# Kernel tuning notes

Measured on AMD Instinct MI355X. Metric: run time of the kernel, lower is better.

Reference implementation:

```python
import jax, jax.numpy as jnp
import numpy as np

L_RTN = 3  # complex taps produced by the RTN head (w_rtn3 out dim = 2*L_RTN)
EPS = 1e-12


def _to_complex(x):
    # (B, 2n) real interleaved [re0, im0, re1, im1, ...] -> (B, n) complex
    return x[:, 0::2] + 1j * x[:, 1::2]


def _to_real(xc):
    # (B, n) complex -> (B, 2n) real interleaved
    b, n = xc.shape
    return jnp.stack([xc.real, xc.imag], axis=-1).reshape(b, 2 * n)


def _complex_conv_taps(h_c, x_c):
    # per-sample causal complex FIR: out[t] = sum_l h[l] * x[t-l]
    # h_c: (B, L) complex, x_c: (B, n) complex
    n = x_c.shape[1]
    out = jnp.zeros_like(x_c)
    for l in range(h_c.shape[1]):  # L is tiny and static
        shifted = jnp.pad(x_c, ((0, 0), (l, 0)))[:, :n]
        out = out + h_c[:, l:l + 1] * shifted
    return out


def setup_inputs() -> dict:
    key = jax.random.key(0)
    ks = jax.random.split(key, 16)
    B, D_IN, H1, CH, H_RTN, H2, D_OUT = 8192, 512, 4096, 256, 1024, 4096, 512
    s = 0.02  # weight init scale
    x = jax.random.normal(ks[0], (B, D_IN), jnp.float32)
    w1 = s * jax.random.normal(ks[1], (H1, D_IN), jnp.float32)
    b1 = jnp.zeros((H1,), jnp.float32)
    w2 = s * jax.random.normal(ks[2], (CH, H1), jnp.float32)
    b2 = jnp.zeros((CH,), jnp.float32)
    w_rtn1 = s * jax.random.normal(ks[3], (H_RTN, CH), jnp.float32)
    b_rtn1 = jnp.zeros((H_RTN,), jnp.float32)
    w_rtn2 = s * jax.random.normal(ks[4], (H_RTN, H_RTN), jnp.float32)
    b_rtn2 = jnp.zeros((H_RTN,), jnp.float32)
    w_rtn3 = s * jax.random.normal(ks[5], (2 * L_RTN, H_RTN), jnp.float32)
    # bias so that RTN starts near identity tap [1, 0, 0, ...]
    b_rtn3 = jnp.zeros((2 * L_RTN,), jnp.float32).at[0].set(1.0)
    w3 = s * jax.random.normal(ks[6], (H2, CH), jnp.float32)
    b3 = jnp.zeros((H2,), jnp.float32)
    w4 = s * jax.random.normal(ks[7], (D_OUT, H2), jnp.float32)
    b4 = jnp.zeros((D_OUT,), jnp.float32)
    h = jax.random.normal(ks[8], (2,), jnp.float32)
    h = h / jnp.linalg.norm(h)  # unit-power single-tap fading channel
    noise = 0.1 * jax.random.normal(ks[9], (B, CH), jnp.float32)
    return {"x": x, "w1": w1, "b1": b1, "w2": w2, "b2": b2,
            "w_rtn1": w_rtn1, "b_rtn1": b_rtn1, "w_rtn2": w_rtn2,
            "b_rtn2": b_rtn2, "w_rtn3": w_rtn3, "b_rtn3": b_rtn3,
            "w3": w3, "b3": b3, "w4": w4, "b4": b4, "h": h, "noise": noise}


def reference(x, w1, b1, w2, b2, w_rtn1, b_rtn1, w_rtn2, b_rtn2,
              w_rtn3, b_rtn3, w3, b3, w4, b4, h, noise):
    # encoder (linear1 -> relu -> linear2)
    a = jax.nn.relu(x @ w1.T + b1)
    s = a @ w2.T + b2                      # (B, 2n) channel signal
    # power normalization: sqrt(2n) * sqrt(0.5) * s / ||s||
    scale = jnp.sqrt(s.shape[1] * 0.5)
    s = scale * s / jnp.linalg.norm(s, axis=1, keepdims=True)
    tx_c = _to_complex(s)                  # (B, n) transmitted symbols
    # single-tap complex channel
    h_c = h[0] + 1j * h[1]
    y = _to_real(h_c * tx_c) + noise       # add per-sample AWGN
    y_c = _to_complex(y)
    # LS channel estimate (1 tap): h_est = <y, x> / <x, x>
    num = jnp.sum(y_c * jnp.conj(tx_c), axis=1, keepdims=True)
    den = jnp.sum(jnp.abs(tx_c) ** 2, axis=1, keepdims=True)
    h_est = num / den                      # (B, 1)
    # zero-forcing signal estimate
    x_eq = y_c * jnp.conj(h_est) / (jnp.abs(h_est) ** 2 + EPS)
    xr = _to_real(x_eq)                    # (B, 2n)
    # RTN: predict inverse taps and apply per-sample complex conv
    g = jnp.tanh(xr @ w_rtn1.T + b_rtn1)
    g = jnp.tanh(g @ w_rtn2.T + b_rtn2)
    h_inv = g @ w_rtn3.T + b_rtn3          # (B, 2*L_RTN)
    h_inv_c = h_inv[:, 0::2] + 1j * h_inv[:, 1::2]
    xr = _to_real(_complex_conv_taps(h_inv_c, _to_complex(xr)))
    # decoder (linear3 -> relu -> linear4)
    out = jax.nn.relu(xr @ w3.T + b3)
    return out @ w4.T + b4
```

## Files before the change

### kernel.cpp

```cpp
#include <hip/hip_runtime.h>
#include <hip/hip_bf16.h>
#include <math.h>

using bf16 = __hip_bfloat16;
typedef __attribute__((ext_vector_type(8))) short short8;
typedef __attribute__((ext_vector_type(4))) float float4v;

template <typename T> __device__ inline T cvt_out(float v);
template <> __device__ inline float cvt_out<float>(float v) { return v; }
template <> __device__ inline bf16 cvt_out<bf16>(float v) { return __float2bfloat16(v); }

__device__ inline void gload_lds16(const bf16* g, bf16* l) {
    __builtin_amdgcn_global_load_lds(
        (const __attribute__((address_space(1))) void*)g,
        (__attribute__((address_space(3))) void*)l, 16, 0, 0);
}

struct CvtPack {
    const float* src[7];
    bf16* dst[7];
    int end[7];
};

__global__ __launch_bounds__(256) void cvt_all(CvtPack p) {
    int e = (blockIdx.x * 256 + threadIdx.x) * 4;
    int start = 0;
#pragma unroll
    for (int s = 0; s < 7; ++s) {
        if (e < p.end[s]) {
            int off = e - start;
            float4 v = *(const float4*)(p.src[s] + off);
            bf16* d = p.dst[s] + off;
            d[0] = __float2bfloat16(v.x);
            d[1] = __float2bfloat16(v.y);
            d[2] = __float2bfloat16(v.z);
            d[3] = __float2bfloat16(v.w);
            return;
        }
        start = p.end[s];
    }
}

template <int NK>
__global__ __launch_bounds__(256) void reduceK_bias(const float* __restrict__ p,
                                                    const float* __restrict__ bias,
                                                    float* __restrict__ out,
                                                    size_t mn, int nmask, int total4) {
    int i = blockIdx.x * 256 + threadIdx.x;
    if (i < total4) {
        int idx = i * 4;
        float4 bb = *(const float4*)(bias + (idx & nmask));
        float4 r = bb;
#pragma unroll
        for (int k = 0; k < NK; ++k) {
            float4 a = *(const float4*)(p + k * mn + idx);
            r.x += a.x; r.y += a.y; r.z += a.z; r.w += a.w;
        }
        *(float4*)(out + idx) = r;
    }
}

template <int ACT, typename OutT, int WMT, int WNT, int BKT, bool PARTIAL>
__global__ __launch_bounds__(256) void gemm_bt(const bf16* __restrict__ A,
                                               const bf16* __restrict__ W,
                                               const float* __restrict__ bias,
                                               OutT* __restrict__ C,
                                               int M, int N, int K,
                                               int nbn, int kcount) {
    constexpr int TBM = 32 * WMT;
    constexpr int TBN = 32 * WNT;
    constexpr int CPR = BKT / 8;
    constexpr int CA = TBM * CPR;
    constexpr int CB = TBN * CPR;
    constexpr int STAGE_B = (TBM + TBN) * BKT * 2;
    constexpr int REPACK_B = TBM * TBN * (int)sizeof(OutT);
    constexpr int SH = STAGE_B > REPACK_B ? STAGE_B : REPACK_B;

    __shared__ __align__(16) char smem[SH];
    bf16* As = (bf16*)smem;
    bf16* Bs = As + TBM * BKT;

    const int bi = blockIdx.x;
    const int xcd = bi & 7, t = bi >> 3;
    const int bn = t % nbn;
    const int bm = xcd + 8 * (t / nbn);
    const int kbeg = PARTIAL ? blockIdx.y * kcount : 0;
    OutT* Cp = PARTIAL ? C + (size_t)blockIdx.y * M * N : C;

    const int tid = threadIdx.x;
    const int wave = tid >> 6, lane = tid & 63;
    const int wm = (wave >> 1) * (16 * WMT), wn = (wave & 1) * (16 * WNT);
    const int quad = lane >> 4, lrow = lane & 15;

    float4v acc[WMT][WNT] = {};
    const size_t arow = (size_t)(bm * TBM) * K;
    const size_t brow = (size_t)(bn * TBN) * K;

    for (int k0 = kbeg; k0 < kbeg + kcount; k0 += BKT) {
        __syncthreads();
#pragma unroll
        for (int tt = 0; tt < CA / 256; ++tt) {
            int base = tt * 256 + wave * 64;
            int c = base + lane;
            int row = c / CPR, col = (c % CPR) * 8;
            gload_lds16(A + arow + (size_t)row * K + k0 + col, As + base * 8);
        }
#pragma unroll
        for (int tt = 0; tt < CB / 256; ++tt) {
            int base = tt * 256 + wave * 64;
            int c = base + lane;
            int row = c / CPR, col = (c % CPR) * 8;
            gload_lds16(W + brow + (size_t)row * K + k0 + col, Bs + base * 8);
        }
        __syncthreads();
#pragma unroll
        for (int kk = 0; kk < BKT; kk += 32) {
            short8 af[WMT], bfr[WNT];
#pragma unroll
            for (int i = 0; i < WMT; ++i)
                af[i] = *(const short8*)(As + (wm + i * 16 + lrow) * BKT + kk + quad * 8);
#pragma unroll
            for (int j = 0; j < WNT; ++j)
                bfr[j] = *(const short8*)(Bs + (wn + j * 16 + lrow) * BKT + kk + quad * 8);
#pragma unroll
            for (int i = 0; i < WMT; ++i)
#pragma unroll
                for (int j = 0; j < WNT; ++j)
                    acc[i][j] = __builtin_amdgcn_mfma_f32_16x16x32_bf16(af[i], bfr[j], acc[i][j], 0, 0, 0);
        }
    }

    __syncthreads();
    OutT* R = (OutT*)smem;
#pragma unroll
    for (int i = 0; i < WMT; ++i) {
        int row0 = wm + i * 16 + quad * 4;
#pragma unroll
        for (int j = 0; j < WNT; ++j) {
            int col = wn + j * 16 + lrow;
            float bv = 0.f;
            if constexpr (!PARTIAL) bv = bias[bn * TBN + col];
#pragma unroll
            for (int r = 0; r < 4; ++r) {
                float v = acc[i][j][r] + bv;
                if constexpr (!PARTIAL) {
                    if (ACT == 1) v = fmaxf(v, 0.f);
                    else if (ACT == 2) v = tanhf(v);
                }
                R[(row0 + r) * TBN + col] = cvt_out<OutT>(v);
            }
        }
    }
    __syncthreads();
    constexpr int EPC = 16 / (int)sizeof(OutT);
    constexpr int CR = TBN / EPC;
    constexpr int TOT = TBM * CR;
#pragma unroll
    for (int t2 = 0; t2 < TOT / 256; ++t2) {
        int c = t2 * 256 + tid;
        int row = c / CR, cin = c % CR;
        float4 v = *((const float4*)smem + c);
        *(float4*)&Cp[(size_t)(bm * TBM + row) * N + bn * TBN + cin * EPC] = v;
    }
}

__global__ __launch_bounds__(64) void channel_kernel(const float* __restrict__ s,
                                                     const float* __restrict__ h,
                                                     const float* __restrict__ noise,
                                                     float* __restrict__ xr_f,
                                                     bf16* __restrict__ xr_b) {
    const int b = blockIdx.x, lane = threadIdx.x;
    const float* srow = s + (size_t)b * 256;

    float ss = 0.f;
#pragma unroll
    for (int t = 0; t < 4; ++t) {
        float v = srow[lane + 64 * t];
        ss += v * v;
    }
#pragma unroll
    for (int off = 32; off; off >>= 1) ss += __shfl_xor(ss, off);
    const float inv = sqrtf(128.0f) / sqrtf(ss);

    const float hre = h[0], him = h[1];

    float yre[2], yim[2];
    float nre = 0.f, nim = 0.f, den = 0.f;
#pragma unroll
    for (int t = 0; t < 2; ++t) {
        int c = lane + 64 * t;
        float tr = srow[2 * c] * inv, ti = srow[2 * c + 1] * inv;
        float yr = hre * tr - him * ti + noise[(size_t)b * 256 + 2 * c];
        float yi = hre * ti + him * tr + noise[(size_t)b * 256 + 2 * c + 1];
        yre[t] = yr; yim[t] = yi;
        nre += yr * tr + yi * ti;
        nim += yi * tr - yr * ti;
        den += tr * tr + ti * ti;
    }
#pragma unroll
    for (int off = 32; off; off >>= 1) {
        nre += __shfl_xor(nre, off);
        nim += __shfl_xor(nim, off);
        den += __shfl_xor(den, off);
    }
    const float her = nre / den, hei = nim / den;
    const float d2 = her * her + hei * hei + 1e-12f;

#pragma unroll
    for (int t = 0; t < 2; ++t) {
        int c = lane + 64 * t;
        float xre = (yre[t] * her + yim[t] * hei) / d2;
        float xim = (yim[t] * her - yre[t] * hei) / d2;
        xr_f[(size_t)b * 256 + 2 * c] = xre;
        xr_f[(size_t)b * 256 + 2 * c + 1] = xim;
        xr_b[(size_t)b * 256 + 2 * c] = __float2bfloat16(xre);
        xr_b[(size_t)b * 256 + 2 * c + 1] = __float2bfloat16(xim);
    }
}

__global__ __launch_bounds__(64) void rtn_taps_conv(const bf16* __restrict__ g2,
                                                    const float* __restrict__ wr3,
                                                    const float* __restrict__ br3,
                                                    const float* __restrict__ xr_f,
                                                    bf16* __restrict__ xr2) {
    const int b = blockIdx.x, lane = threadIdx.x;
    const bf16* grow = g2 + (size_t)b * 1024;

    float acc[6] = {0.f, 0.f, 0.f, 0.f, 0.f, 0.f};
#pragma unroll
    for (int t = 0; t < 16; ++t) {
        int k = lane + 64 * t;
        float gv = __bfloat162float(grow[k]);
#pragma unroll
        for (int j = 0; j < 6; ++j) acc[j] += gv * wr3[j * 1024 + k];
    }
#pragma unroll
    for (int j = 0; j < 6; ++j)
#pragma unroll
        for (int off = 32; off; off >>= 1) acc[j] += __shfl_xor(acc[j], off);

    float tre[3], tim[3];
#pragma unroll
    for (int l = 0; l < 3; ++l) {
        tre[l] = acc[2 * l] + br3[2 * l];
        tim[l] = acc[2 * l + 1] + br3[2 * l + 1];
    }

    const float* xrow = xr_f + (size_t)b * 256;
#pragma unroll
    for (int t = 0; t < 2; ++t) {
        int c = lane + 64 * t;
        float ore = 0.f, oim = 0.f;
#pragma unroll
        for (int l = 0; l < 3; ++l) {
            int cc = c - l;
            if (cc >= 0) {
                float xre = xrow[2 * cc], xim = xrow[2 * cc + 1];
                ore += tre[l] * xre - tim[l] * xim;
                oim += tre[l] * xim + tim[l] * xre;
            }
        }
        xr2[(size_t)b * 256 + 2 * c] = __float2bfloat16(ore);
        xr2[(size_t)b * 256 + 2 * c + 1] = __float2bfloat16(oim);
    }
}

extern "C" void kernel_launch(void* const* d_in, const int* in_sizes, int n_in,
                              void* d_out, int out_size, void* d_ws, size_t ws_size,
                              hipStream_t stream) {
    constexpr int B = 8192, D_IN = 512, H1 = 4096, CH = 256, HR = 1024, H2 = 4096, DOUT = 512;

    const float* x   = (const float*)d_in[0];
    const float* w1  = (const float*)d_in[1];
    const float* b1  = (const float*)d_in[2];
    const float* w2  = (const float*)d_in[3];
    const float* b2  = (const float*)d_in[4];
    const float* wr1 = (const float*)d_in[5];
    const float* br1 = (const float*)d_in[6];
    const float* wr2 = (const float*)d_in[7];
    const float* br2 = (const float*)d_in[8];
    const float* wr3 = (const float*)d_in[9];
    const float* br3 = (const float*)d_in[10];
    const float* w3  = (const float*)d_in[11];
    const float* b3  = (const float*)d_in[12];
    const float* w4  = (const float*)d_in[13];
    const float* b4  = (const float*)d_in[14];
    const float* h   = (const float*)d_in[15];
    const float* noise = (const float*)d_in[16];

    char* ws = (char*)d_ws;
    bf16*  a    = (bf16*)(ws + 0);
    bf16*  g1   = (bf16*)(ws + 0);
    bf16*  g2   = (bf16*)(ws + 16777216);
    bf16*  tbuf = (bf16*)(ws + 0);
    bf16*  w1B  = (bf16*)(ws + 67108864);
    bf16*  w2B  = (bf16*)(ws + 71303168);
    bf16*  wr1B = (bf16*)(ws + 73400320);
    bf16*  wr2B = (bf16*)(ws + 73924608);
    bf16*  w3B  = (bf16*)(ws + 76021760);
    bf16*  w4B  = (bf16*)(ws + 78118912);
    bf16*  xB   = (bf16*)(ws + 82313216);
    float* sF   = (float*)(ws + 90701824);
    float* xrF  = (float*)(ws + 99090432);
    bf16*  xrB  = (bf16*)(ws + 107479040);
    bf16*  xr2  = (bf16*)(ws + 111673344);

    float* g2P = (float*)(ws + 82313216);
    float* g6P = (float*)(ws + 82313216);

    dim3 blk(256);

    CvtPack p;
    const float* srcs[7] = {x, w1, w2, wr1, wr2, w3, w4};
    bf16* dsts[7] = {xB, w1B, w2B, wr1B, wr2B, w3B, w4B};
    int ns[7] = {B * D_IN, H1 * D_IN, CH * H1, HR * CH, HR * HR, H2 * CH, DOUT * H2};
    int cum = 0;
    for (int i = 0; i < 7; ++i) { p.src[i] = srcs[i]; p.dst[i] = dsts[i]; cum += ns[i]; p.end[i] = cum; }
    cvt_all<<<(cum / 4 + 255) / 256, blk, 0, stream>>>(p);

    gemm_bt<1, bf16, 4, 4, 64, false><<<64 * 32, blk, 0, stream>>>(
        xB, w1B, b1, a, B, H1, D_IN, 32, D_IN);
    gemm_bt<0, float, 4, 2, 64, true><<<dim3(64 * 4, 4), blk, 0, stream>>>(
        a, w2B, nullptr, g2P, B, CH, H1, 4, H1 / 4);
    reduceK_bias<4><<<(B * CH / 4 + 255) / 256, blk, 0, stream>>>(
        g2P, b2, sF, (size_t)B * CH, CH - 1, B * CH / 4);
    channel_kernel<<<B, 64, 0, stream>>>(sF, h, noise, xrF, xrB);
    gemm_bt<2, bf16, 4, 2, 64, false><<<64 * 16, blk, 0, stream>>>(
        xrB, wr1B, br1, g1, B, HR, CH, 16, CH);
    gemm_bt<2, bf16, 4, 2, 64, false><<<64 * 16, blk, 0, stream>>>(
        g1, wr2B, br2, g2, B, HR, HR, 16, HR);
    rtn_taps_conv<<<B, 64, 0, stream>>>(g2, wr3, br3, xrF, xr2);
    gemm_bt<1, bf16, 4, 4, 64, false><<<64 * 32, blk, 0, stream>>>(
        xr2, w3B, b3, tbuf, B, H2, CH, 32, CH);
    gemm_bt<0, float, 4, 2, 64, true><<<dim3(64 * 8, 2), blk, 0, stream>>>(
        tbuf, w4B, nullptr, g6P, B, DOUT, H2, 8, H2 / 2);
    reduceK_bias<2><<<(B * DOUT / 4 + 255) / 256, blk, 0, stream>>>(
        g6P, b4, (float*)d_out, (size_t)B * DOUT, DOUT - 1, B * DOUT / 4);
}
```

Baseline: 387.9 us.

## Add 512-thread 256x128 GEMM kernel and drop LDS-staged epilogue

Adds a wide GEMM kernel with 8 waves computing a 256x128 tile and uses it for the two large ReLU layers (w1 and w3). The aim is more reuse of each LDS-staged tile and fewer blocks. Separately, the epilogue in the generic GEMM no longer repacks results through shared memory for coalesced 16-byte stores; it writes scalar elements straight from the accumulators. That saves an LDS round trip and a barrier but risks poorly coalesced global stores, especially for the bf16 and float partial outputs.

After: 369.2 us. 1.05x faster.

```diff
diff --git a/kernel.cpp b/kernel.cpp
--- a/kernel.cpp
+++ b/kernel.cpp
@@ -72,13 +72,9 @@
     constexpr int CPR = BKT / 8;
     constexpr int CA = TBM * CPR;
     constexpr int CB = TBN * CPR;
-    constexpr int STAGE_B = (TBM + TBN) * BKT * 2;
-    constexpr int REPACK_B = TBM * TBN * (int)sizeof(OutT);
-    constexpr int SH = STAGE_B > REPACK_B ? STAGE_B : REPACK_B;
-
-    __shared__ __align__(16) char smem[SH];
-    bf16* As = (bf16*)smem;
-    bf16* Bs = As + TBM * BKT;
+
+    __shared__ bf16 As[TBM * BKT];
+    __shared__ bf16 Bs[TBN * BKT];
 
     const int bi = blockIdx.x;
     const int xcd = bi & 7, t = bi >> 3;
@@ -130,37 +126,108 @@
         }
     }
 
-    __syncthreads();
-    OutT* R = (OutT*)smem;
 #pragma unroll
     for (int i = 0; i < WMT; ++i) {
-        int row0 = wm + i * 16 + quad * 4;
+        int m0 = bm * TBM + wm + i * 16 + quad * 4;
 #pragma unroll
         for (int j = 0; j < WNT; ++j) {
-            int col = wn + j * 16 + lrow;
-            float bv = 0.f;
-            if constexpr (!PARTIAL) bv = bias[bn * TBN + col];
+            int n = bn * TBN + wn + j * 16 + lrow;
+            if constexpr (PARTIAL) {
+#pragma unroll
+                for (int r = 0; r < 4; ++r)
+                    Cp[(size_t)(m0 + r) * N + n] = acc[i][j][r];
+            } else {
+                float bv = bias[n];
+#pragma unroll
+                for (int r = 0; r < 4; ++r) {
+                    float v = acc[i][j][r] + bv;
+                    if (ACT == 1) v = fmaxf(v, 0.f);
+                    else if (ACT == 2) v = tanhf(v);
+                    Cp[(size_t)(m0 + r) * N + n] = cvt_out<OutT>(v);
+                }
+            }
+        }
+    }
+}
+
+template <int ACT, typename OutT>
+__global__ __launch_bounds__(512, 4) void gemm_bt_wide(const bf16* __restrict__ A,
+                                                       const bf16* __restrict__ W,
+                                                       const float* __restrict__ bias,
+                                                       OutT* __restrict__ C,
+                                                       int M, int N, int K,
+                                                       int nbn) {
+    constexpr int TBM = 256, TBN = 128, BKT = 64;
+    constexpr int CPR = BKT / 8;
+    constexpr int CA = TBM * CPR;
+    constexpr int CB = TBN * CPR;
+
+    __shared__ bf16 As[TBM * BKT];
+    __shared__ bf16 Bs[TBN * BKT];
+
+    const int bi = blockIdx.x;
+    const int xcd = bi & 7, t = bi >> 3;
+    const int bn = t % nbn;
+    const int bm = xcd + 8 * (t / nbn);
+
+    const int tid = threadIdx.x;
+    const int wave = tid >> 6, lane = tid & 63;
+    const int wm = (wave >> 1) * 64, wn = (wave & 1) * 64;
+    const int quad = lane >> 4, lrow = lane & 15;
+
+    float4v acc[4][4] = {};
+    const size_t arow = (size_t)(bm * TBM) * K;
+    const size_t brow = (size_t)(bn * TBN) * K;
+
+    for (int k0 = 0; k0 < K; k0 += BKT) {
+        __syncthreads();
+#pragma unroll
+        for (int tt = 0; tt < CA / 512; ++tt) {
+            int base = tt * 512 + wave * 64;
+            int c = base + lane;
+            int row = c / CPR, col = (c % CPR) * 8;
+            gload_lds16(A + arow + (size_t)row * K + k0 + col, As + base * 8);
+        }
+#pragma unroll
+        for (int tt = 0; tt < CB / 512; ++tt) {
+            int base = tt * 512 + wave * 64;
+            int c = base + lane;
+            int row = c / CPR, col = (c % CPR) * 8;
+            gload_lds16(W + brow + (size_t)row * K + k0 + col, Bs + base * 8);
+        }
+        __syncthreads();
+#pragma unroll
+        for (int kk = 0; kk < BKT; kk += 32) {
+            short8 af[4], bfr[4];
+#pragma unroll
+            for (int i = 0; i < 4; ++i)
+                af[i] = *(const short8*)(As + (wm + i * 16 + lrow) * BKT + kk + quad * 8);
+#pragma unroll
+            for (int j = 0; j < 4; ++j)
+                bfr[j] = *(const short8*)(Bs + (wn + j * 16 + lrow) * BKT + kk + quad * 8);
+#pragma unroll
+            for (int i = 0; i < 4; ++i)
+#pragma unroll
+                for (int j = 0; j < 4; ++j)
+                    acc[i][j] = __builtin_amdgcn_mfma_f32_16x16x32_bf16(af[i], bfr[j], acc[i][j], 0, 0, 0);
+        }
+    }
+
+#pragma unroll
+    for (int i = 0; i < 4; ++i) {
+        int m0 = bm * TBM + wm + i * 16 + quad * 4;
+#pragma unroll
+        for (int j = 0; j < 4; ++j) {
+            int n = bn * TBN + wn + j * 16 + lrow;
+            float bv = bias[n];
 #pragma unroll
             for (int r = 0; r < 4; ++r) {
                 float v = acc[i][j][r] + bv;
-                if constexpr (!PARTIAL) {
-                    if (ACT == 1) v = fmaxf(v, 0.f);
-                    else if (ACT == 2) v = tanhf(v);
-                }
-                R[(row0 + r) * TBN + col] = cvt_out<OutT>(v);
+                if (ACT == 1) v = fmaxf(v, 0.f);
+                else if (ACT == 2) v = tanhf(v);
+                C[(size_t)(m0 + r) * N + n] = cvt_out<OutT>(v);
             }
         }
-    }
-    __syncthreads();
-    constexpr int EPC = 16 / (int)sizeof(OutT);
-    constexpr int CR = TBN / EPC;
-    constexpr int TOT = TBM * CR;
-#pragma unroll
-    for (int t2 = 0; t2 < TOT / 256; ++t2) {
-        int c = t2 * 256 + tid;
-        int row = c / CR, cin = c % CR;
-        float4 v = *((const float4*)smem + c);
-        *(float4*)&Cp[(size_t)(bm * TBM + row) * N + bn * TBN + cin * EPC] = v;
     }
 }
 
@@ -318,8 +385,8 @@
     for (int i = 0; i < 7; ++i) { p.src[i] = srcs[i]; p.dst[i] = dsts[i]; cum += ns[i]; p.end[i] = cum; }
     cvt_all<<<(cum / 4 + 255) / 256, blk, 0, stream>>>(p);
 
-    gemm_bt<1, bf16, 4, 4, 64, false><<<64 * 32, blk, 0, stream>>>(
-        xB, w1B, b1, a, B, H1, D_IN, 32, D_IN);
+    gemm_bt_wide<1, bf16><<<32 * 32, dim3(512), 0, stream>>>(
+        xB, w1B, b1, a, B, H1, D_IN, 32);
     gemm_bt<0, float, 4, 2, 64, true><<<dim3(64 * 4, 4), blk, 0, stream>>>(
         a, w2B, nullptr, g2P, B, CH, H1, 4, H1 / 4);
     reduceK_bias<4><<<(B * CH / 4 + 255) / 256, blk, 0, stream>>>(
@@ -330,8 +397,8 @@
     gemm_bt<2, bf16, 4, 2, 64, false><<<64 * 16, blk, 0, stream>>>(
         g1, wr2B, br2, g2, B, HR, HR, 16, HR);
     rtn_taps_conv<<<B, 64, 0, stream>>>(g2, wr3, br3, xrF, xr2);
-    gemm_bt<1, bf16, 4, 4, 64, false><<<64 * 32, blk, 0, stream>>>(
-        xr2, w3B, b3, tbuf, B, H2, CH, 32, CH);
+    gemm_bt_wide<1, bf16><<<32 * 32, dim3(512), 0, stream>>>(
+        xr2, w3B, b3, tbuf, B, H2, CH, 32);
     gemm_bt<0, float, 4, 2, 64, true><<<dim3(64 * 8, 2), blk, 0, stream>>>(
         tbuf, w4B, nullptr, g6P, B, DOUT, H2, 8, H2 / 2);
     reduceK_bias<2><<<(B * DOUT / 4 + 255) / 256, blk, 0, stream>>>(
```
